# Kernel tuning notes

Measured on AMD Instinct MI355X. Metric: run time of the kernel, lower is better.

## Reference

```python
import jax, jax.numpy as jnp
import numpy as np

EPS = 1e-7  # keras.backend.epsilon()
B, U, F = 1024, 256, 31
D = 1 + U + F  # features dim after concat


def setup_inputs() -> dict:
    key = jax.random.key(0)
    ks = jax.random.split(key, 9)
    s = 1.0 / np.sqrt(D)
    return {
        "last_cell": jax.random.uniform(ks[0], (B, U), dtype=jnp.float32),
        "input_precipitation": jax.random.uniform(ks[1], (B,), dtype=jnp.float32),
        "input_other_features": jax.random.normal(ks[2], (B, F), dtype=jnp.float32),
        "W_i": jax.random.normal(ks[3], (D, U), dtype=jnp.float32) * s,
        "b_i": jnp.zeros((U,), dtype=jnp.float32),
        "W_r": jax.random.normal(ks[4], (D, U * U), dtype=jnp.float32) * s,
        "b_r": jnp.zeros((U * U,), dtype=jnp.float32),
        "W_o": jax.random.normal(ks[5], (D, U), dtype=jnp.float32) * s,
        "b_o": jnp.zeros((U,), dtype=jnp.float32),
    }


def reference(last_cell, input_precipitation, input_other_features,
              W_i, b_i, W_r, b_r, W_o, b_o):
    # L1-normalize last cell state (mass fractions)
    l1 = jnp.sum(jnp.abs(last_cell), axis=-1, keepdims=True) + EPS
    last_cell_hat = last_cell / l1
    p = input_precipitation[:, None]  # [B,1]
    features = jnp.concatenate([p, last_cell_hat, input_other_features], axis=-1)  # [B,D]

    # input gate: sigmoid then L1-normalized across units (mass-conserving split)
    ig = jax.nn.sigmoid(features @ W_i + b_i)
    ig = ig / jnp.sum(jnp.abs(ig), axis=-1, keepdims=True)

    # redistribution matrix: relu, reshape [B,U,U], L1-normalize each row
    R = jax.nn.relu(features @ W_r + b_r).reshape(-1, U, U)
    R = R / jnp.sum(jnp.abs(R), axis=-1, keepdims=True)

    # output gate: sigmoid
    og = jax.nn.sigmoid(features @ W_o + b_o)

    cell_in = ig * p                                   # [B,U]
    cell_sys = jnp.einsum('bu,buv->bv', last_cell, R)  # batched (1xU)@(UxU)
    candidate = cell_in + cell_sys
    output = og * candidate
    cell = (1.0 - og) * candidate
    return (cell, output)
```

## Files before the change

### kernel.cpp

```cpp
#include <hip/hip_runtime.h>


#define EPS_L1 1e-7f

constexpr int B = 1024;
constexpr int U = 256;
constexpr int F = 31;
constexpr int D = 1 + U + F;
constexpr int NBV = B * U;
constexpr int NCH = D / 32;
constexpr int UIMGB = NCH * 16384;
constexpr size_t WTB_BYTES  = (size_t)258 * UIMGB;
constexpr size_t FEAT_BYTES = (size_t)B * D * 2;

typedef float f32x4 __attribute__((ext_vector_type(4)));
typedef short bf16x8 __attribute__((ext_vector_type(8)));

__device__ __forceinline__ unsigned short f2bf(float x) {
  union { float f; unsigned u; } v; v.f = x;
  unsigned r = v.u + 0x7FFFu + ((v.u >> 16) & 1u);
  return (unsigned short)(r >> 16);
}

#define GLDS16(gp, lp)                                                        \
  __builtin_amdgcn_global_load_lds(                                          \
      (const __attribute__((address_space(1))) void*)(gp),                   \
      (__attribute__((address_space(3))) void*)(lp), 16, 0, 0)

__global__ __launch_bounds__(256) void k_wtA(
    const float* __restrict__ Wr, const float* __restrict__ Wi,
    const float* __restrict__ Wo, short* __restrict__ WtB) {
  __shared__ short lds[32 * 258];
  const int t = threadIdx.x;
  const int u = blockIdx.x / 9;
  const int c = blockIdx.x % 9;
  const int k0 = c * 32;

  const float* src; long ld;
  if (u < 256)       { src = Wr + (size_t)u * 256; ld = 65536; }
  else if (u == 256) { src = Wi; ld = 256; }
  else               { src = Wo; ld = 256; }

#pragma unroll
  for (int i = 0; i < 8; ++i) {
    const int r = i * 4 + (t >> 6);
    const int col = (t & 63) * 4;
    const float4 v = *(const float4*)(src + (size_t)(k0 + r) * ld + col);
    const unsigned lo = (unsigned)f2bf(v.x) | ((unsigned)f2bf(v.y) << 16);
    const unsigned hi = (unsigned)f2bf(v.z) | ((unsigned)f2bf(v.w) << 16);
    *(unsigned*)&lds[r * 258 + col]     = lo;
    *(unsigned*)&lds[r * 258 + col + 2] = hi;
  }
  __syncthreads();

#pragma unroll
  for (int i = 0; i < 4; ++i) {
    const int n0 = i * 4 + (t >> 6);
    const int l = t & 63;
    const int g = l >> 4, l15 = l & 15;
    bf16x8 h;
#pragma unroll
    for (int j = 0; j < 8; ++j)
      h[j] = lds[(g * 8 + j) * 258 + n0 * 16 + l15];
    *(bf16x8*)(WtB + (size_t)u * 73728 + (size_t)(c * 16 + n0) * 512 + l * 8) = h;
  }
}

__global__ __launch_bounds__(256) void k_featA(
    const float* __restrict__ lc, const float* __restrict__ p,
    const float* __restrict__ other, short* __restrict__ featImg) {
  __shared__ float inv_s[64];
  const int t = threadIdx.x, b0 = blockIdx.x * 64;
  const int row = t >> 2, q = t & 3;
  const float4* lp = (const float4*)(lc + (size_t)(b0 + row) * 256 + q * 64);
  float s = 0.f;
#pragma unroll
  for (int j = 0; j < 16; ++j) {
    const float4 v = lp[j];
    s += fabsf(v.x) + fabsf(v.y) + fabsf(v.z) + fabsf(v.w);
  }
  s += __shfl_xor(s, 1, 64);
  s += __shfl_xor(s, 2, 64);
  if (q == 0) inv_s[row] = 1.f / (s + EPS_L1);
  __syncthreads();

#pragma unroll
  for (int i = 0; i < 9; ++i) {
    const int idx = i * 256 + t;
    const int reg = idx >> 6, l = idx & 63;
    const int c = reg >> 2, mt = reg & 3;
    const int lrow = mt * 16 + (l & 15);
    const int grow = b0 + lrow;
    const int k0 = c * 32 + (l >> 4) * 8;
    bf16x8 h;
#pragma unroll
    for (int j = 0; j < 8; ++j) {
      const int k = k0 + j;
      float v;
      if (k == 0) v = p[grow];
      else if (k <= 256) v = lc[(size_t)grow * 256 + (k - 1)] * inv_s[lrow];
      else v = other[(size_t)grow * 31 + (k - 257)];
      h[j] = (short)f2bf(v);
    }
    *(bf16x8*)(featImg + (size_t)blockIdx.x * 18432 + (size_t)reg * 512 + l * 8) = h;
  }
}

__global__ __launch_bounds__(512, 4) void k_heavyM2(
    const short* __restrict__ featImg, const short* __restrict__ WtB,
    const float* __restrict__ lc, const float* __restrict__ br,
    float* __restrict__ cell_sys) {
  __shared__ short aT[18432];
  __shared__ float rsum[2][64][12];
  __shared__ float lcs[2][64];

  const int t = threadIdx.x, lane = t & 63, cg = t >> 6;
  const int quad = lane >> 4, l15 = lane & 15;
  const int bid = blockIdx.x;
  const int ug = (bid & 7) * 4 + ((bid >> 3) >> 4);
  const int mb = (bid >> 3) & 15;
  const int b0 = mb * 64;
  const int u0 = ug * 8;

  {
    const char* gsrc = (const char*)featImg + (size_t)mb * 36864;
    char* ldst = (char*)aT;
#pragma unroll
    for (int i = 0; i < 5; ++i) {
      if (i * 8 + cg < 36) {
        const int off = i * 8192 + t * 16;
        GLDS16(gsrc + off, ldst + off);
      }
    }
  }

  f32x4 acc[4][2], outa[4][2];
#pragma unroll
  for (int mt = 0; mt < 4; ++mt)
#pragma unroll
    for (int n = 0; n < 2; ++n)
#pragma unroll
      for (int r = 0; r < 4; ++r) { acc[mt][n][r] = 0.f; outa[mt][n][r] = 0.f; }

  const char* bptr = (const char*)WtB + (size_t)u0 * UIMGB + cg * 2048 + lane * 16;
  bf16x8 cb0 = *(const bf16x8*)(bptr);
  bf16x8 cb1 = *(const bf16x8*)(bptr + 1024);
  bf16x8 nb0 = *(const bf16x8*)(bptr + 16384);
  bf16x8 nb1 = *(const bf16x8*)(bptr + 16384 + 1024);
  bptr += 32768;

  __syncthreads();

  float lcreg = 0.f, bv0 = 0.f, bv1 = 0.f;

  for (int uu = 0; uu < 8; ++uu) {
#pragma unroll
    for (int c = 0; c < 9; ++c) {
      const bf16x8 pb0 = *(const bf16x8*)(bptr);
      const bf16x8 pb1 = *(const bf16x8*)(bptr + 1024);
      bptr += 16384;
      if (c == 0) {
        if (t < 64) lcreg = lc[(size_t)(b0 + t) * 256 + u0 + uu];
        bv0 = br[(size_t)(u0 + uu) * 256 + cg * 32 + l15];
        bv1 = br[(size_t)(u0 + uu) * 256 + cg * 32 + 16 + l15];
      }
      const char* ab = (const char*)aT + c * 4096 + lane * 16;
      const bf16x8 a0 = *(const bf16x8*)(ab);
      const bf16x8 a1 = *(const bf16x8*)(ab + 1024);
      const bf16x8 a2 = *(const bf16x8*)(ab + 2048);
      const bf16x8 a3 = *(const bf16x8*)(ab + 3072);
      acc[0][0] = __builtin_amdgcn_mfma_f32_16x16x32_bf16(a0, cb0, acc[0][0], 0, 0, 0);
      acc[0][1] = __builtin_amdgcn_mfma_f32_16x16x32_bf16(a0, cb1, acc[0][1], 0, 0, 0);
      acc[1][0] = __builtin_amdgcn_mfma_f32_16x16x32_bf16(a1, cb0, acc[1][0], 0, 0, 0);
      acc[1][1] = __builtin_amdgcn_mfma_f32_16x16x32_bf16(a1, cb1, acc[1][1], 0, 0, 0);
      acc[2][0] = __builtin_amdgcn_mfma_f32_16x16x32_bf16(a2, cb0, acc[2][0], 0, 0, 0);
      acc[2][1] = __builtin_amdgcn_mfma_f32_16x16x32_bf16(a2, cb1, acc[2][1], 0, 0, 0);
      acc[3][0] = __builtin_amdgcn_mfma_f32_16x16x32_bf16(a3, cb0, acc[3][0], 0, 0, 0);
      acc[3][1] = __builtin_amdgcn_mfma_f32_16x16x32_bf16(a3, cb1, acc[3][1], 0, 0, 0);
      cb0 = nb0; cb1 = nb1; nb0 = pb0; nb1 = pb1;
    }

    {
      const int ub = uu & 1;
      float sm[4][4];
#pragma unroll
      for (int mt = 0; mt < 4; ++mt)
#pragma unroll
        for (int r = 0; r < 4; ++r)
          sm[mt][r] = fmaxf(acc[mt][0][r] + bv0, 0.f) + fmaxf(acc[mt][1][r] + bv1, 0.f);
#pragma unroll
      for (int m = 1; m < 16; m <<= 1)
#pragma unroll
        for (int mt = 0; mt < 4; ++mt)
#pragma unroll
          for (int r = 0; r < 4; ++r)
            sm[mt][r] += __shfl_xor(sm[mt][r], m, 64);
      if (l15 == 0) {
#pragma unroll
        for (int mt = 0; mt < 4; ++mt)
#pragma unroll
          for (int r = 0; r < 4; ++r)
            rsum[ub][mt * 16 + quad * 4 + r][cg] = sm[mt][r];
      }
      if (t < 64) lcs[ub][t] = lcreg;
      __syncthreads();
#pragma unroll
      for (int mt = 0; mt < 4; ++mt)
#pragma unroll
        for (int r = 0; r < 4; ++r) {
          const int row = mt * 16 + quad * 4 + r;
          const float4 ra = *(const float4*)&rsum[ub][row][0];
          const float4 rb = *(const float4*)&rsum[ub][row][4];
          const float rs = ((ra.x + ra.y) + (ra.z + ra.w)) + ((rb.x + rb.y) + (rb.z + rb.w));
          const float alpha = lcs[ub][row] / rs;
          outa[mt][0][r] = fmaf(alpha, fmaxf(acc[mt][0][r] + bv0, 0.f), outa[mt][0][r]);
          outa[mt][1][r] = fmaf(alpha, fmaxf(acc[mt][1][r] + bv1, 0.f), outa[mt][1][r]);
          acc[mt][0][r] = 0.f;
          acc[mt][1][r] = 0.f;
        }
    }
  }

#pragma unroll
  for (int mt = 0; mt < 4; ++mt)
#pragma unroll
    for (int r = 0; r < 4; ++r) {
      const int grow = b0 + mt * 16 + quad * 4 + r;
#pragma unroll
      for (int n = 0; n < 2; ++n)
        atomicAdd(&cell_sys[(size_t)grow * 256 + cg * 32 + n * 16 + l15],
                  outa[mt][n][r]);
    }
}

__global__ __launch_bounds__(512, 4) void k_gatesM2(
    const short* __restrict__ featImg, const short* __restrict__ WtB,
    const float* __restrict__ bi, const float* __restrict__ bo,
    float* __restrict__ dout) {
  __shared__ short aT[18432];
  __shared__ float rsum[64][12];

  const int t = threadIdx.x, lane = t & 63, cg = t >> 6;
  const int quad = lane >> 4, l15 = lane & 15;
  const int mb = blockIdx.x, b0 = mb * 64;

  {
    const char* gsrc = (const char*)featImg + (size_t)mb * 36864;
    char* ldst = (char*)aT;
#pragma unroll
    for (int i = 0; i < 5; ++i) {
      if (i * 8 + cg < 36) {
        const int off = i * 8192 + t * 16;
        GLDS16(gsrc + off, ldst + off);
      }
    }
  }

  f32x4 acc[4][2];
#pragma unroll
  for (int mt = 0; mt < 4; ++mt)
#pragma unroll
    for (int n = 0; n < 2; ++n)
#pragma unroll
      for (int r = 0; r < 4; ++r) acc[mt][n][r] = 0.f;

  const char* bptr = (const char*)WtB + (size_t)256 * UIMGB + cg * 2048 + lane * 16;
  bf16x8 cb0 = *(const bf16x8*)(bptr);
  bf16x8 cb1 = *(const bf16x8*)(bptr + 1024);
  bf16x8 nb0 = *(const bf16x8*)(bptr + 16384);
  bf16x8 nb1 = *(const bf16x8*)(bptr + 16384 + 1024);
  bptr += 32768;

  __syncthreads();

#pragma unroll
  for (int g = 0; g < 2; ++g) {
    const float* bias = (g == 0) ? bi : bo;
    const float bv0 = bias[cg * 32 + l15];
    const float bv1 = bias[cg * 32 + 16 + l15];
#pragma unroll
    for (int c = 0; c < 9; ++c) {
      const bf16x8 pb0 = *(const bf16x8*)(bptr);
      const bf16x8 pb1 = *(const bf16x8*)(bptr + 1024);
      bptr += 16384;
      const char* ab = (const char*)aT + c * 4096 + lane * 16;
      const bf16x8 a0 = *(const bf16x8*)(ab);
      const bf16x8 a1 = *(const bf16x8*)(ab + 1024);
      const bf16x8 a2 = *(const bf16x8*)(ab + 2048);
      const bf16x8 a3 = *(const bf16x8*)(ab + 3072);
      acc[0][0] = __builtin_amdgcn_mfma_f32_16x16x32_bf16(a0, cb0, acc[0][0], 0, 0, 0);
      acc[0][1] = __builtin_amdgcn_mfma_f32_16x16x32_bf16(a0, cb1, acc[0][1], 0, 0, 0);
      acc[1][0] = __builtin_amdgcn_mfma_f32_16x16x32_bf16(a1, cb0, acc[1][0], 0, 0, 0);
      acc[1][1] = __builtin_amdgcn_mfma_f32_16x16x32_bf16(a1, cb1, acc[1][1], 0, 0, 0);
      acc[2][0] = __builtin_amdgcn_mfma_f32_16x16x32_bf16(a2, cb0, acc[2][0], 0, 0, 0);
      acc[2][1] = __builtin_amdgcn_mfma_f32_16x16x32_bf16(a2, cb1, acc[2][1], 0, 0, 0);
      acc[3][0] = __builtin_amdgcn_mfma_f32_16x16x32_bf16(a3, cb0, acc[3][0], 0, 0, 0);
      acc[3][1] = __builtin_amdgcn_mfma_f32_16x16x32_bf16(a3, cb1, acc[3][1], 0, 0, 0);
      cb0 = nb0; cb1 = nb1; nb0 = pb0; nb1 = pb1;
    }

    float s0[4][4], s1[4][4];
#pragma unroll
    for (int mt = 0; mt < 4; ++mt)
#pragma unroll
      for (int r = 0; r < 4; ++r) {
        s0[mt][r] = 1.f / (1.f + __expf(-(acc[mt][0][r] + bv0)));
        s1[mt][r] = 1.f / (1.f + __expf(-(acc[mt][1][r] + bv1)));
        acc[mt][0][r] = 0.f;
        acc[mt][1][r] = 0.f;
      }

    if (g == 0) {
      float sm[4][4];
#pragma unroll
      for (int mt = 0; mt < 4; ++mt)
#pragma unroll
        for (int r = 0; r < 4; ++r) sm[mt][r] = s0[mt][r] + s1[mt][r];
#pragma unroll
      for (int m = 1; m < 16; m <<= 1)
#pragma unroll
        for (int mt = 0; mt < 4; ++mt)
#pragma unroll
          for (int r = 0; r < 4; ++r)
            sm[mt][r] += __shfl_xor(sm[mt][r], m, 64);
      if (l15 == 0) {
#pragma unroll
        for (int mt = 0; mt < 4; ++mt)
#pragma unroll
          for (int r = 0; r < 4; ++r)
            rsum[mt * 16 + quad * 4 + r][cg] = sm[mt][r];
      }
      __syncthreads();
#pragma unroll
      for (int mt = 0; mt < 4; ++mt)
#pragma unroll
        for (int r = 0; r < 4; ++r) {
          const int row = mt * 16 + quad * 4 + r;
          const float4 ra = *(const float4*)&rsum[row][0];
          const float4 rb = *(const float4*)&rsum[row][4];
          const float inv = 1.f / (((ra.x + ra.y) + (ra.z + ra.w)) +
                                   ((rb.x + rb.y) + (rb.z + rb.w)));
          dout[(size_t)(b0 + row) * 256 + cg * 32 + l15]      = s0[mt][r] * inv;
          dout[(size_t)(b0 + row) * 256 + cg * 32 + 16 + l15] = s1[mt][r] * inv;
        }
    } else {
#pragma unroll
      for (int mt = 0; mt < 4; ++mt)
#pragma unroll
        for (int r = 0; r < 4; ++r) {
          const int row = mt * 16 + quad * 4 + r;
          dout[(size_t)NBV + (size_t)(b0 + row) * 256 + cg * 32 + l15]      = s0[mt][r];
          dout[(size_t)NBV + (size_t)(b0 + row) * 256 + cg * 32 + 16 + l15] = s1[mt][r];
        }
    }
  }
}

__global__ __launch_bounds__(256) void k_final(
    const float* __restrict__ cell_sys, const float* __restrict__ p,
    float* __restrict__ d_out) {
  const int i = blockIdx.x * 256 + threadIdx.x;
  const float ig = d_out[i];
  const float ogv = d_out[NBV + i];
  const float cand = fmaf(ig, p[i >> 8], cell_sys[i]);
  const float outp = ogv * cand;
  d_out[i] = (1.0f - ogv) * cand;
  d_out[NBV + i] = outp;
}

extern "C" void kernel_launch(void* const* d_in, const int* in_sizes, int n_in,
                              void* d_out, int out_size, void* d_ws, size_t ws_size,
                              hipStream_t stream) {
  const float* lc    = (const float*)d_in[0];
  const float* p     = (const float*)d_in[1];
  const float* other = (const float*)d_in[2];
  const float* bi    = (const float*)d_in[4];
  const float* Wr    = (const float*)d_in[5];
  const float* br    = (const float*)d_in[6];
  const float* Wi    = (const float*)d_in[3];
  const float* Wo    = (const float*)d_in[7];
  const float* bo    = (const float*)d_in[8];
  float* out = (float*)d_out;

  char* wsb = (char*)d_ws;
  short* WtB      = (short*)wsb;
  short* featImg  = (short*)(wsb + WTB_BYTES);
  float* cell_sys = (float*)(wsb + WTB_BYTES + FEAT_BYTES);

  hipMemsetAsync(cell_sys, 0, (size_t)NBV * sizeof(float), stream);
  k_wtA<<<258 * 9, 256, 0, stream>>>(Wr, Wi, Wo, WtB);
  k_featA<<<16, 256, 0, stream>>>(lc, p, other, featImg);
  k_gatesM2<<<16, 512, 0, stream>>>(featImg, WtB, bi, bo, out);
  k_heavyM2<<<512, 512, 0, stream>>>(featImg, WtB, lc, br, cell_sys);
  k_final<<<1024, 256, 0, stream>>>(cell_sys, p, out);
}
```

Measured before the change: 234.9 us.

## Merge prep kernels, retile heavy GEMM to 128 rows, fuse gates with final epilogue

Weight conversion, feature packing and the cell_sys zeroing now run in one launch: 258 blocks for weights, 16 for features and 8 for zeroing. The heavy redistribution GEMM is retiled so each block covers 128 batch rows and 8 units with 8 N-tiles per wave, which doubles A reuse and cuts W_r reads. The gate kernel now runs after the heavy kernel and also does the final combine, so the separate final kernel and the round trip of the gate values through global memory are gone. Risks: the weight-prep blocks are now serial per unit, with far fewer blocks than before. Running gates after the heavy kernel puts them on the critical path with only 16 blocks, and the larger per-thread tile raises register pressure.

```diff
diff --git a/kernel.cpp b/kernel.cpp
--- a/kernel.cpp
+++ b/kernel.cpp
@@ -3,23 +3,24 @@
 
 #define EPS_L1 1e-7f
 
-constexpr int B = 1024;
-constexpr int U = 256;
-constexpr int F = 31;
-constexpr int D = 1 + U + F;
-constexpr int NBV = B * U;
+constexpr int BB  = 1024;
+constexpr int U   = 256;
+constexpr int F   = 31;
+constexpr int D   = 1 + U + F;
+constexpr int NBV = BB * U;
 constexpr int NCH = D / 32;
 constexpr int UIMGB = NCH * 16384;
 constexpr size_t WTB_BYTES  = (size_t)258 * UIMGB;
-constexpr size_t FEAT_BYTES = (size_t)B * D * 2;
+constexpr size_t FEAT_BYTES = (size_t)BB * D * 2;
+constexpr int PITCH = 260;
 
 typedef float f32x4 __attribute__((ext_vector_type(4)));
 typedef short bf16x8 __attribute__((ext_vector_type(8)));
 
-__device__ __forceinline__ unsigned short f2bf(float x) {
+__device__ __forceinline__ unsigned f2bf(float x) {
   union { float f; unsigned u; } v; v.f = x;
   unsigned r = v.u + 0x7FFFu + ((v.u >> 16) & 1u);
-  return (unsigned short)(r >> 16);
+  return r >> 16;
 }
 
 #define GLDS16(gp, lp)                                                        \
@@ -27,234 +28,250 @@
       (const __attribute__((address_space(1))) void*)(gp),                   \
       (__attribute__((address_space(3))) void*)(lp), 16, 0, 0)
 
-__global__ __launch_bounds__(256) void k_wtA(
-    const float* __restrict__ Wr, const float* __restrict__ Wi,
-    const float* __restrict__ Wo, short* __restrict__ WtB) {
-  __shared__ short lds[32 * 258];
-  const int t = threadIdx.x;
-  const int u = blockIdx.x / 9;
-  const int c = blockIdx.x % 9;
-  const int k0 = c * 32;
-
-  const float* src; long ld;
-  if (u < 256)       { src = Wr + (size_t)u * 256; ld = 65536; }
-  else if (u == 256) { src = Wi; ld = 256; }
-  else               { src = Wo; ld = 256; }
-
-#pragma unroll
-  for (int i = 0; i < 8; ++i) {
-    const int r = i * 4 + (t >> 6);
-    const int col = (t & 63) * 4;
-    const float4 v = *(const float4*)(src + (size_t)(k0 + r) * ld + col);
-    const unsigned lo = (unsigned)f2bf(v.x) | ((unsigned)f2bf(v.y) << 16);
-    const unsigned hi = (unsigned)f2bf(v.z) | ((unsigned)f2bf(v.w) << 16);
-    *(unsigned*)&lds[r * 258 + col]     = lo;
-    *(unsigned*)&lds[r * 258 + col + 2] = hi;
-  }
-  __syncthreads();
-
-#pragma unroll
-  for (int i = 0; i < 4; ++i) {
-    const int n0 = i * 4 + (t >> 6);
-    const int l = t & 63;
-    const int g = l >> 4, l15 = l & 15;
-    bf16x8 h;
-#pragma unroll
-    for (int j = 0; j < 8; ++j)
-      h[j] = lds[(g * 8 + j) * 258 + n0 * 16 + l15];
-    *(bf16x8*)(WtB + (size_t)u * 73728 + (size_t)(c * 16 + n0) * 512 + l * 8) = h;
+__global__ __launch_bounds__(256) void k_prep(
+    const float* __restrict__ lc, const float* __restrict__ p,
+    const float* __restrict__ other,
+    const float* __restrict__ Wi, const float* __restrict__ Wr,
+    const float* __restrict__ Wo,
+    short* __restrict__ WtB, short* __restrict__ featImg,
+    float* __restrict__ cell_sys) {
+  __shared__ short lds[2][32 * PITCH];
+  __shared__ float inv_s[64];
+  const int bid = blockIdx.x, t = threadIdx.x;
+
+  if (bid < 258) {
+    const float* src; long ld;
+    if (bid < 256)       { src = Wr + (size_t)bid * 256; ld = 65536; }
+    else if (bid == 256) { src = Wi; ld = 256; }
+    else                 { src = Wo; ld = 256; }
+    short* dst = WtB + (size_t)bid * 73728;
+    const int lane = t & 63, wave = t >> 6;
+    const int g = lane >> 4, l15 = lane & 15;
+
+    for (int c = 0; c < 9; ++c) {
+      short* buf = lds[c & 1];
+#pragma unroll
+      for (int i = 0; i < 8; ++i) {
+        const int f = i * 256 + t;
+        const int row = f >> 6, col4 = f & 63;
+        const float4 v = *(const float4*)(src + (size_t)(c * 32 + row) * ld + col4 * 4);
+        const unsigned lo = f2bf(v.x) | (f2bf(v.y) << 16);
+        const unsigned hi = f2bf(v.z) | (f2bf(v.w) << 16);
+        unsigned* wp = (unsigned*)&buf[row * PITCH + col4 * 4];
+        wp[0] = lo; wp[1] = hi;
+      }
+      __syncthreads();
+#pragma unroll
+      for (int i = 0; i < 4; ++i) {
+        const int n0 = wave * 4 + i;
+        bf16x8 h;
+#pragma unroll
+        for (int j = 0; j < 8; ++j)
+          h[j] = buf[(g * 8 + j) * PITCH + n0 * 16 + l15];
+        *(bf16x8*)(dst + (size_t)(c * 16 + n0) * 512 + lane * 8) = h;
+      }
+    }
+  } else if (bid < 274) {
+    const int mb = bid - 258;
+    const int b0 = mb * 64;
+    const int row = t >> 2, q = t & 3;
+    const float4* lp = (const float4*)(lc + (size_t)(b0 + row) * 256 + q * 64);
+    float s = 0.f;
+#pragma unroll
+    for (int j = 0; j < 16; ++j) {
+      const float4 v = lp[j];
+      s += fabsf(v.x) + fabsf(v.y) + fabsf(v.z) + fabsf(v.w);
+    }
+    s += __shfl_xor(s, 1, 64);
+    s += __shfl_xor(s, 2, 64);
+    if (q == 0) inv_s[row] = 1.f / (s + EPS_L1);
+    __syncthreads();
+#pragma unroll
+    for (int i = 0; i < 9; ++i) {
+      const int idx = i * 256 + t;
+      const int reg = idx >> 6, l = idx & 63;
+      const int c = reg >> 2, mt = reg & 3;
+      const int lrow = mt * 16 + (l & 15);
+      const int grow = b0 + lrow;
+      const int k0 = c * 32 + (l >> 4) * 8;
+      bf16x8 h;
+#pragma unroll
+      for (int j = 0; j < 8; ++j) {
+        const int k = k0 + j;
+        float v;
+        if (k == 0) v = p[grow];
+        else if (k <= 256) v = lc[(size_t)grow * 256 + (k - 1)] * inv_s[lrow];
+        else v = other[(size_t)grow * 31 + (k - 257)];
+        h[j] = (short)f2bf(v);
+      }
+      *(bf16x8*)(featImg + (size_t)mb * 18432 + (size_t)reg * 512 + l * 8) = h;
+    }
+  } else {
+    float4* cs4 = (float4*)cell_sys;
+    const int base = (bid - 274) * 8192 + t;
+    const float4 z = {0.f, 0.f, 0.f, 0.f};
+#pragma unroll
+    for (int k2 = 0; k2 < 32; ++k2) cs4[base + k2 * 256] = z;
   }
 }
 
-__global__ __launch_bounds__(256) void k_featA(
-    const float* __restrict__ lc, const float* __restrict__ p,
-    const float* __restrict__ other, short* __restrict__ featImg) {
-  __shared__ float inv_s[64];
-  const int t = threadIdx.x, b0 = blockIdx.x * 64;
-  const int row = t >> 2, q = t & 3;
-  const float4* lp = (const float4*)(lc + (size_t)(b0 + row) * 256 + q * 64);
-  float s = 0.f;
-#pragma unroll
-  for (int j = 0; j < 16; ++j) {
-    const float4 v = lp[j];
-    s += fabsf(v.x) + fabsf(v.y) + fabsf(v.z) + fabsf(v.w);
-  }
-  s += __shfl_xor(s, 1, 64);
-  s += __shfl_xor(s, 2, 64);
-  if (q == 0) inv_s[row] = 1.f / (s + EPS_L1);
-  __syncthreads();
-
-#pragma unroll
-  for (int i = 0; i < 9; ++i) {
-    const int idx = i * 256 + t;
-    const int reg = idx >> 6, l = idx & 63;
-    const int c = reg >> 2, mt = reg & 3;
-    const int lrow = mt * 16 + (l & 15);
-    const int grow = b0 + lrow;
-    const int k0 = c * 32 + (l >> 4) * 8;
-    bf16x8 h;
-#pragma unroll
-    for (int j = 0; j < 8; ++j) {
-      const int k = k0 + j;
-      float v;
-      if (k == 0) v = p[grow];
-      else if (k <= 256) v = lc[(size_t)grow * 256 + (k - 1)] * inv_s[lrow];
-      else v = other[(size_t)grow * 31 + (k - 257)];
-      h[j] = (short)f2bf(v);
-    }
-    *(bf16x8*)(featImg + (size_t)blockIdx.x * 18432 + (size_t)reg * 512 + l * 8) = h;
-  }
-}
-
-__global__ __launch_bounds__(512, 4) void k_heavyM2(
+__global__ __launch_bounds__(512, 2) void k_heavyR4(
     const short* __restrict__ featImg, const short* __restrict__ WtB,
     const float* __restrict__ lc, const float* __restrict__ br,
     float* __restrict__ cell_sys) {
+  __shared__ short aT[36864];
+  __shared__ float rsum[2][2][128];
+  __shared__ float lcs[2][128];
+
+  const int t = threadIdx.x, lane = t & 63, wave = t >> 6;
+  const int rg = wave >> 1, cg = wave & 1;
+  const int quad = lane >> 4, l15 = lane & 15;
+  const int bid = blockIdx.x;
+  const int Mb = bid >> 5, ug = bid & 31;
+  const int b0 = Mb * 128, u0 = ug * 8;
+
+  {
+    const char* gA = (const char*)featImg + (size_t)Mb * 73728;
+    char* lA = (char*)aT;
+#pragma unroll
+    for (int i = 0; i < 9; ++i)
+      GLDS16(gA + i * 8192 + t * 16, lA + i * 8192 + t * 16);
+  }
+
+  const char* bptr = (const char*)WtB + (size_t)u0 * UIMGB + cg * 8192 + lane * 16;
+  bf16x8 bc[8], bn[8];
+#pragma unroll
+  for (int n = 0; n < 8; ++n) bc[n] = *(const bf16x8*)(bptr + n * 1024);
+  bptr += 16384;
+
+  f32x4 acc[2][8], outa[2][8];
+#pragma unroll
+  for (int mt = 0; mt < 2; ++mt)
+#pragma unroll
+    for (int n = 0; n < 8; ++n)
+#pragma unroll
+      for (int r = 0; r < 4; ++r) { acc[mt][n][r] = 0.f; outa[mt][n][r] = 0.f; }
+
+  const char* aB = (const char*)aT + (rg >> 1) * 36864 + (rg & 1) * 2048 + lane * 16;
+
+  __syncthreads();
+
+  bf16x8 a0 = *(const bf16x8*)(aB);
+  bf16x8 a1 = *(const bf16x8*)(aB + 1024);
+
+  float bv[8], lcv = 0.f;
+  int c = 0, u = u0;
+
+  for (int s = 0; s < 72; ++s) {
+#pragma unroll
+    for (int n = 0; n < 8; ++n) bn[n] = *(const bf16x8*)(bptr + n * 1024);
+    bptr += 16384;
+    if (c == 0) {
+#pragma unroll
+      for (int n = 0; n < 8; ++n)
+        bv[n] = br[(size_t)u * 256 + cg * 128 + n * 16 + l15];
+      if (t < 128) lcv = lc[(size_t)(b0 + t) * 256 + u];
+    }
+    const int cn = (c == 8) ? 0 : c + 1;
+    const bf16x8 an0 = *(const bf16x8*)(aB + cn * 4096);
+    const bf16x8 an1 = *(const bf16x8*)(aB + cn * 4096 + 1024);
+
+#pragma unroll
+    for (int n = 0; n < 8; ++n) {
+      acc[0][n] = __builtin_amdgcn_mfma_f32_16x16x32_bf16(a0, bc[n], acc[0][n], 0, 0, 0);
+      acc[1][n] = __builtin_amdgcn_mfma_f32_16x16x32_bf16(a1, bc[n], acc[1][n], 0, 0, 0);
+    }
+    a0 = an0; a1 = an1;
+#pragma unroll
+    for (int n = 0; n < 8; ++n) bc[n] = bn[n];
+
+    if (c == 8) {
+      const int ub = u & 1;
+      float sm[2][4];
+#pragma unroll
+      for (int mt = 0; mt < 2; ++mt)
+#pragma unroll
+        for (int r = 0; r < 4; ++r) {
+          float sv = 0.f;
+#pragma unroll
+          for (int n = 0; n < 8; ++n) {
+            const float rv = fmaxf(acc[mt][n][r] + bv[n], 0.f);
+            acc[mt][n][r] = rv;
+            sv += rv;
+          }
+          sm[mt][r] = sv;
+        }
+#pragma unroll
+      for (int m = 1; m < 16; m <<= 1)
+#pragma unroll
+        for (int mt = 0; mt < 2; ++mt)
+#pragma unroll
+          for (int r = 0; r < 4; ++r)
+            sm[mt][r] += __shfl_xor(sm[mt][r], m, 64);
+      if (l15 == 0) {
+#pragma unroll
+        for (int mt = 0; mt < 2; ++mt)
+#pragma unroll
+          for (int r = 0; r < 4; ++r)
+            rsum[ub][cg][rg * 32 + mt * 16 + quad * 4 + r] = sm[mt][r];
+      }
+      if (t < 128) lcs[ub][t] = lcv;
+      __syncthreads();
+#pragma unroll
+      for (int mt = 0; mt < 2; ++mt)
+#pragma unroll
+        for (int r = 0; r < 4; ++r) {
+          const int row = rg * 32 + mt * 16 + quad * 4 + r;
+          const float alpha = lcs[ub][row] / (rsum[ub][0][row] + rsum[ub][1][row]);
+#pragma unroll
+          for (int n = 0; n < 8; ++n) {
+            outa[mt][n][r] = fmaf(alpha, acc[mt][n][r], outa[mt][n][r]);
+            acc[mt][n][r] = 0.f;
+          }
+        }
+      c = 0; ++u;
+    } else {
+      ++c;
+    }
+  }
+
+#pragma unroll
+  for (int mt = 0; mt < 2; ++mt)
+#pragma unroll
+    for (int r = 0; r < 4; ++r) {
+      const int grow = b0 + rg * 32 + mt * 16 + quad * 4 + r;
+#pragma unroll
+      for (int n = 0; n < 8; ++n)
+        atomicAdd(&cell_sys[(size_t)grow * 256 + cg * 128 + n * 16 + l15],
+                  outa[mt][n][r]);
+    }
+}
+
+__global__ __launch_bounds__(512, 2) void k_post(
+    const short* __restrict__ featImg, const short* __restrict__ WtB,
+    const float* __restrict__ bi, const float* __restrict__ bo,
+    const float* __restrict__ p, const float* __restrict__ cell_sys,
+    float* __restrict__ dout) {
   __shared__ short aT[18432];
-  __shared__ float rsum[2][64][12];
-  __shared__ float lcs[2][64];
+  __shared__ float rsum[64][12];
+  __shared__ float ps[64];
 
   const int t = threadIdx.x, lane = t & 63, cg = t >> 6;
   const int quad = lane >> 4, l15 = lane & 15;
-  const int bid = blockIdx.x;
-  const int ug = (bid & 7) * 4 + ((bid >> 3) >> 4);
-  const int mb = (bid >> 3) & 15;
-  const int b0 = mb * 64;
-  const int u0 = ug * 8;
+  const int mb = blockIdx.x, b0 = mb * 64;
 
   {
     const char* gsrc = (const char*)featImg + (size_t)mb * 36864;
-    char* ldst = (char*)aT;
+    char* lbase = (char*)aT;
 #pragma unroll
     for (int i = 0; i < 5; ++i) {
       if (i * 8 + cg < 36) {
         const int off = i * 8192 + t * 16;
-        GLDS16(gsrc + off, ldst + off);
+        GLDS16(gsrc + off, lbase + off);
       }
     }
   }
-
-  f32x4 acc[4][2], outa[4][2];
-#pragma unroll
-  for (int mt = 0; mt < 4; ++mt)
-#pragma unroll
-    for (int n = 0; n < 2; ++n)
-#pragma unroll
-      for (int r = 0; r < 4; ++r) { acc[mt][n][r] = 0.f; outa[mt][n][r] = 0.f; }
-
-  const char* bptr = (const char*)WtB + (size_t)u0 * UIMGB + cg * 2048 + lane * 16;
-  bf16x8 cb0 = *(const bf16x8*)(bptr);
-  bf16x8 cb1 = *(const bf16x8*)(bptr + 1024);
-  bf16x8 nb0 = *(const bf16x8*)(bptr + 16384);
-  bf16x8 nb1 = *(const bf16x8*)(bptr + 16384 + 1024);
-  bptr += 32768;
-
-  __syncthreads();
-
-  float lcreg = 0.f, bv0 = 0.f, bv1 = 0.f;
-
-  for (int uu = 0; uu < 8; ++uu) {
-#pragma unroll
-    for (int c = 0; c < 9; ++c) {
-      const bf16x8 pb0 = *(const bf16x8*)(bptr);
-      const bf16x8 pb1 = *(const bf16x8*)(bptr + 1024);
-      bptr += 16384;
-      if (c == 0) {
-        if (t < 64) lcreg = lc[(size_t)(b0 + t) * 256 + u0 + uu];
-        bv0 = br[(size_t)(u0 + uu) * 256 + cg * 32 + l15];
-        bv1 = br[(size_t)(u0 + uu) * 256 + cg * 32 + 16 + l15];
-      }
-      const char* ab = (const char*)aT + c * 4096 + lane * 16;
-      const bf16x8 a0 = *(const bf16x8*)(ab);
-      const bf16x8 a1 = *(const bf16x8*)(ab + 1024);
-      const bf16x8 a2 = *(const bf16x8*)(ab + 2048);
-      const bf16x8 a3 = *(const bf16x8*)(ab + 3072);
-      acc[0][0] = __builtin_amdgcn_mfma_f32_16x16x32_bf16(a0, cb0, acc[0][0], 0, 0, 0);
-      acc[0][1] = __builtin_amdgcn_mfma_f32_16x16x32_bf16(a0, cb1, acc[0][1], 0, 0, 0);
-      acc[1][0] = __builtin_amdgcn_mfma_f32_16x16x32_bf16(a1, cb0, acc[1][0], 0, 0, 0);
-      acc[1][1] = __builtin_amdgcn_mfma_f32_16x16x32_bf16(a1, cb1, acc[1][1], 0, 0, 0);
-      acc[2][0] = __builtin_amdgcn_mfma_f32_16x16x32_bf16(a2, cb0, acc[2][0], 0, 0, 0);
-      acc[2][1] = __builtin_amdgcn_mfma_f32_16x16x32_bf16(a2, cb1, acc[2][1], 0, 0, 0);
-      acc[3][0] = __builtin_amdgcn_mfma_f32_16x16x32_bf16(a3, cb0, acc[3][0], 0, 0, 0);
-      acc[3][1] = __builtin_amdgcn_mfma_f32_16x16x32_bf16(a3, cb1, acc[3][1], 0, 0, 0);
-      cb0 = nb0; cb1 = nb1; nb0 = pb0; nb1 = pb1;
-    }
-
-    {
-      const int ub = uu & 1;
-      float sm[4][4];
-#pragma unroll
-      for (int mt = 0; mt < 4; ++mt)
-#pragma unroll
-        for (int r = 0; r < 4; ++r)
-          sm[mt][r] = fmaxf(acc[mt][0][r] + bv0, 0.f) + fmaxf(acc[mt][1][r] + bv1, 0.f);
-#pragma unroll
-      for (int m = 1; m < 16; m <<= 1)
-#pragma unroll
-        for (int mt = 0; mt < 4; ++mt)
-#pragma unroll
-          for (int r = 0; r < 4; ++r)
-            sm[mt][r] += __shfl_xor(sm[mt][r], m, 64);
-      if (l15 == 0) {
-#pragma unroll
-        for (int mt = 0; mt < 4; ++mt)
-#pragma unroll
-          for (int r = 0; r < 4; ++r)
-            rsum[ub][mt * 16 + quad * 4 + r][cg] = sm[mt][r];
-      }
-      if (t < 64) lcs[ub][t] = lcreg;
-      __syncthreads();
-#pragma unroll
-      for (int mt = 0; mt < 4; ++mt)
-#pragma unroll
-        for (int r = 0; r < 4; ++r) {
-          const int row = mt * 16 + quad * 4 + r;
-          const float4 ra = *(const float4*)&rsum[ub][row][0];
-          const float4 rb = *(const float4*)&rsum[ub][row][4];
-          const float rs = ((ra.x + ra.y) + (ra.z + ra.w)) + ((rb.x + rb.y) + (rb.z + rb.w));
-          const float alpha = lcs[ub][row] / rs;
-          outa[mt][0][r] = fmaf(alpha, fmaxf(acc[mt][0][r] + bv0, 0.f), outa[mt][0][r]);
-          outa[mt][1][r] = fmaf(alpha, fmaxf(acc[mt][1][r] + bv1, 0.f), outa[mt][1][r]);
-          acc[mt][0][r] = 0.f;
-          acc[mt][1][r] = 0.f;
-        }
-    }
-  }
-
-#pragma unroll
-  for (int mt = 0; mt < 4; ++mt)
-#pragma unroll
-    for (int r = 0; r < 4; ++r) {
-      const int grow = b0 + mt * 16 + quad * 4 + r;
-#pragma unroll
-      for (int n = 0; n < 2; ++n)
-        atomicAdd(&cell_sys[(size_t)grow * 256 + cg * 32 + n * 16 + l15],
-                  outa[mt][n][r]);
-    }
-}
-
-__global__ __launch_bounds__(512, 4) void k_gatesM2(
-    const short* __restrict__ featImg, const short* __restrict__ WtB,
-    const float* __restrict__ bi, const float* __restrict__ bo,
-    float* __restrict__ dout) {
-  __shared__ short aT[18432];
-  __shared__ float rsum[64][12];
-
-  const int t = threadIdx.x, lane = t & 63, cg = t >> 6;
-  const int quad = lane >> 4, l15 = lane & 15;
-  const int mb = blockIdx.x, b0 = mb * 64;
-
-  {
-    const char* gsrc = (const char*)featImg + (size_t)mb * 36864;
-    char* ldst = (char*)aT;
-#pragma unroll
-    for (int i = 0; i < 5; ++i) {
-      if (i * 8 + cg < 36) {
-        const int off = i * 8192 + t * 16;
-        GLDS16(gsrc + off, ldst + off);
-      }
-    }
-  }
+  if (t < 64) ps[t] = p[b0 + t];
 
   f32x4 acc[4][2];
 #pragma unroll
@@ -272,6 +289,8 @@
   bptr += 32768;
 
   __syncthreads();
+
+  float ig0[4][4], ig1[4][4], og0[4][4], og1[4][4];
 
 #pragma unroll
   for (int g = 0; g < 2; ++g) {
@@ -299,13 +318,14 @@
       cb0 = nb0; cb1 = nb1; nb0 = pb0; nb1 = pb1;
     }
 
-    float s0[4][4], s1[4][4];
 #pragma unroll
     for (int mt = 0; mt < 4; ++mt)
 #pragma unroll
       for (int r = 0; r < 4; ++r) {
-        s0[mt][r] = 1.f / (1.f + __expf(-(acc[mt][0][r] + bv0)));
-        s1[mt][r] = 1.f / (1.f + __expf(-(acc[mt][1][r] + bv1)));
+        const float v0 = 1.f / (1.f + __expf(-(acc[mt][0][r] + bv0)));
+        const float v1 = 1.f / (1.f + __expf(-(acc[mt][1][r] + bv1)));
+        if (g == 0) { ig0[mt][r] = v0; ig1[mt][r] = v1; }
+        else        { og0[mt][r] = v0; og1[mt][r] = v1; }
         acc[mt][0][r] = 0.f;
         acc[mt][1][r] = 0.f;
       }
@@ -315,7 +335,7 @@
 #pragma unroll
       for (int mt = 0; mt < 4; ++mt)
 #pragma unroll
-        for (int r = 0; r < 4; ++r) sm[mt][r] = s0[mt][r] + s1[mt][r];
+        for (int r = 0; r < 4; ++r) sm[mt][r] = ig0[mt][r] + ig1[mt][r];
 #pragma unroll
       for (int m = 1; m < 16; m <<= 1)
 #pragma unroll
@@ -340,32 +360,30 @@
           const float4 rb = *(const float4*)&rsum[row][4];
           const float inv = 1.f / (((ra.x + ra.y) + (ra.z + ra.w)) +
                                    ((rb.x + rb.y) + (rb.z + rb.w)));
-          dout[(size_t)(b0 + row) * 256 + cg * 32 + l15]      = s0[mt][r] * inv;
-          dout[(size_t)(b0 + row) * 256 + cg * 32 + 16 + l15] = s1[mt][r] * inv;
+          ig0[mt][r] *= inv;
+          ig1[mt][r] *= inv;
         }
-    } else {
-#pragma unroll
-      for (int mt = 0; mt < 4; ++mt)
-#pragma unroll
-        for (int r = 0; r < 4; ++r) {
-          const int row = mt * 16 + quad * 4 + r;
-          dout[(size_t)NBV + (size_t)(b0 + row) * 256 + cg * 32 + l15]      = s0[mt][r];
-          dout[(size_t)NBV + (size_t)(b0 + row) * 256 + cg * 32 + 16 + l15] = s1[mt][r];
-        }
     }
   }
-}
-
-__global__ __launch_bounds__(256) void k_final(
-    const float* __restrict__ cell_sys, const float* __restrict__ p,
-    float* __restrict__ d_out) {
-  const int i = blockIdx.x * 256 + threadIdx.x;
-  const float ig = d_out[i];
-  const float ogv = d_out[NBV + i];
-  const float cand = fmaf(ig, p[i >> 8], cell_sys[i]);
-  const float outp = ogv * cand;
-  d_out[i] = (1.0f - ogv) * cand;
-  d_out[NBV + i] = outp;
+
+#pragma unroll
+  for (int mt = 0; mt < 4; ++mt)
+#pragma unroll
+    for (int r = 0; r < 4; ++r) {
+      const int row = mt * 16 + quad * 4 + r;
+      const float pr = ps[row];
+      const size_t base = (size_t)(b0 + row) * 256 + cg * 32 + l15;
+      {
+        const float cand = fmaf(ig0[mt][r], pr, cell_sys[base]);
+        dout[base] = (1.f - og0[mt][r]) * cand;
+        dout[NBV + base] = og0[mt][r] * cand;
+      }
+      {
+        const float cand = fmaf(ig1[mt][r], pr, cell_sys[base + 16]);
+        dout[base + 16] = (1.f - og1[mt][r]) * cand;
+        dout[NBV + base + 16] = og1[mt][r] * cand;
+      }
+    }
 }
 
 extern "C" void kernel_launch(void* const* d_in, const int* in_sizes, int n_in,
@@ -374,10 +392,10 @@
   const float* lc    = (const float*)d_in[0];
   const float* p     = (const float*)d_in[1];
   const float* other = (const float*)d_in[2];
+  const float* Wi    = (const float*)d_in[3];
   const float* bi    = (const float*)d_in[4];
   const float* Wr    = (const float*)d_in[5];
   const float* br    = (const float*)d_in[6];
-  const float* Wi    = (const float*)d_in[3];
   const float* Wo    = (const float*)d_in[7];
   const float* bo    = (const float*)d_in[8];
   float* out = (float*)d_out;
@@ -387,10 +405,7 @@
   short* featImg  = (short*)(wsb + WTB_BYTES);
   float* cell_sys = (float*)(wsb + WTB_BYTES + FEAT_BYTES);
 
-  hipMemsetAsync(cell_sys, 0, (size_t)NBV * sizeof(float), stream);
-  k_wtA<<<258 * 9, 256, 0, stream>>>(Wr, Wi, Wo, WtB);
-  k_featA<<<16, 256, 0, stream>>>(lc, p, other, featImg);
-  k_gatesM2<<<16, 512, 0, stream>>>(featImg, WtB, bi, bo, out);
-  k_heavyM2<<<512, 512, 0, stream>>>(featImg, WtB, lc, br, cell_sys);
-  k_final<<<1024, 256, 0, stream>>>(cell_sys, p, out);
+  k_prep<<<282, 256, 0, stream>>>(lc, p, other, Wi, Wr, Wo, WtB, featImg, cell_sys);
+  k_heavyR4<<<256, 512, 0, stream>>>(featImg, WtB, lc, br, cell_sys);
+  k_post<<<16, 512, 0, stream>>>(featImg, WtB, bi, bo, p, cell_sys, out);
 }
```

Measured after the change: 221.7 us. 1.06x faster.
